# Kernel optimization log

Hardware: AMD Instinct MI355X
Metric: run time of the kernel (lower is better)

The kernel has to match this reference:

```python
import jax, jax.numpy as jnp
import numpy as np

IN_FEATURES = 4096
OUT_FEATURES = 8192
GROUP_SIZE = 16
NUM_GROUPS = IN_FEATURES * OUT_FEATURES // GROUP_SIZE  # 2_097_152


def block_dequantize_2bit(packed, normalization):
    # packed: [G, group_size//4] int32 holding uint8 values; norm: [G, 1] fp16
    shifts = jnp.arange(4, dtype=packed.dtype) * 2  # bit offsets 0,2,4,6
    # unpacked column 4k+i comes from packed column k, bits 2i..2i+1
    u = ((packed[:, :, None] >> shifts) & 3).astype(jnp.float32)  # [G, gs/4, 4]
    u = u.reshape(packed.shape[0], -1)  # [G, group_size]
    norm = normalization.astype(jnp.float32)
    return (u / 3.0) * (2.0 * norm) - norm  # [G, group_size]


def setup_inputs() -> dict:
    key = jax.random.key(0)
    k_x, k_q, k_n, k_b = jax.random.split(key, 4)
    x = jax.random.normal(k_x, (256, IN_FEATURES), dtype=jnp.float32)
    # packed 2-bit weights: random bytes (store as int32 for clean bit ops in jax)
    weight_q2 = jax.random.randint(k_q, (NUM_GROUPS, GROUP_SIZE // 4), 0, 256, dtype=jnp.int32)
    # per-group normalization (abs-max), positive, fp16 as in the module buffer
    weight_norm = (jax.random.uniform(k_n, (NUM_GROUPS, 1), dtype=jnp.float32) * 0.05 + 1e-4).astype(jnp.float16)
    bias = jax.random.normal(k_b, (OUT_FEATURES,), dtype=jnp.float32) * 0.01
    return {"x": x, "weight_q2": weight_q2, "weight_norm": weight_norm, "bias": bias}


def reference(x, weight_q2, weight_norm, bias):
    weight = block_dequantize_2bit(weight_q2, weight_norm).reshape(OUT_FEATURES, IN_FEATURES)
    return jnp.dot(x.astype(jnp.float32), weight.T) + bias
```

## Files before the change

### kernel.cpp

```cpp
#include <hip/hip_runtime.h>
#include <hip/hip_bf16.h>
#include <hip/hip_fp16.h>

#define IN_F   4096
#define OUT_F  8192
#define M_ROWS 256

#define SPLITK 2
#define K_SPL  (IN_F / SPLITK)
#define NIT    (K_SPL / 64)

typedef __attribute__((ext_vector_type(8))) short  short8;
typedef __attribute__((ext_vector_type(4))) float  float4v;

__device__ inline unsigned int pack_bf16(float lo, float hi) {
    return __builtin_amdgcn_perm(__float_as_uint(hi), __float_as_uint(lo), 0x07060302u);
}

__device__ inline int sw_idx(int row, int kchunk) {
    return row * 64 + ((kchunk ^ (row & 7)) << 3);
}

__device__ inline void barrier_no_vmem_drain() {
    asm volatile("s_waitcnt lgkmcnt(0)" ::: "memory");
    __builtin_amdgcn_s_barrier();
    asm volatile("" ::: "memory");
}

__global__ void cvt_x_kernel(const float* __restrict__ x, unsigned short* __restrict__ xb) {
    int i = blockIdx.x * blockDim.x + threadIdx.x;
    if (i < (M_ROWS * IN_F) / 4) {
        float4 v = ((const float4*)x)[i];
        uint2 o;
        o.x = pack_bf16(v.x, v.y);
        o.y = pack_bf16(v.z, v.w);
        ((uint2*)xb)[i] = o;
    }
}

__global__ void init_out_kernel(const float* __restrict__ bias, float* __restrict__ out) {
    int i = blockIdx.x * blockDim.x + threadIdx.x;
    if (i < (M_ROWS * OUT_F) / 4) {
        float4 b = ((const float4*)bias)[i & (OUT_F / 4 - 1)];
        ((float4*)out)[i] = b;
    }
}

__device__ inline void load_a16_f32(const float* __restrict__ p, uint4& o0, uint4& o1) {
    float4 v0 = ((const float4*)p)[0], v1 = ((const float4*)p)[1];
    float4 v2 = ((const float4*)p)[2], v3 = ((const float4*)p)[3];
    o0.x = pack_bf16(v0.x, v0.y); o0.y = pack_bf16(v0.z, v0.w);
    o0.z = pack_bf16(v1.x, v1.y); o0.w = pack_bf16(v1.z, v1.w);
    o1.x = pack_bf16(v2.x, v2.y); o1.y = pack_bf16(v2.z, v2.w);
    o1.z = pack_bf16(v3.x, v3.y); o1.w = pack_bf16(v3.z, v3.w);
}

template <bool XB>
__global__ __launch_bounds__(256, 4) void gemm2bit_kernel(
    const float*           __restrict__ xf,
    const unsigned short*  __restrict__ xb,
    const int*             __restrict__ wq,
    const void*            __restrict__ wnorm,
    float*                 __restrict__ out)
{
    __shared__ unsigned short lds[2][2][64 * 64];

    const int t    = threadIdx.x;
    const int n0   = blockIdx.x * 64;
    const int m0   = blockIdx.y * 64;
    const int kb   = blockIdx.z * K_SPL;
    const int wave = t >> 6;
    const int lane = t & 63;
    const int l15  = lane & 15;
    const int quad = lane >> 4;
    const int wm   = (wave >> 1) * 32;
    const int wn   = (wave & 1) * 32;

    const float cand0 = *(const float*)wnorm;
    const bool  nf32  = (cand0 > 1e-5f && cand0 < 0.1f);

    const int srow = t >> 2;
    const int skc  = t & 3;
    const int c0   = skc * 2;
    const int wO0  = sw_idx(srow, c0);
    const int wO1  = sw_idx(srow, c0 + 1);

    int fa0[2], fa1[2], fb0[2], fb1[2];
#pragma unroll
    for (int kk = 0; kk < 2; ++kk) {
        fa0[kk] = sw_idx(wm +      l15, kk * 4 + quad);
        fa1[kk] = sw_idx(wm + 16 + l15, kk * 4 + quad);
        fb0[kk] = sw_idx(wn +      l15, kk * 4 + quad);
        fb1[kk] = sw_idx(wn + 16 + l15, kk * 4 + quad);
    }

    const int arow = m0 + srow;
    const int brow = n0 + srow;
    const float*          nrmF = (const float*)wnorm;
    const __half*         nrmH = (const __half*)wnorm;

    float4v acc[2][2] = {};

    uint4 aN0, aN1; int4 qN; float nN;
    {
        if (XB) {
            const unsigned short* p = xb + arow * IN_F + kb + skc * 16;
            aN0 = *(const uint4*)p;
            aN1 = *(const uint4*)(p + 8);
        } else {
            load_a16_f32(xf + arow * IN_F + kb + skc * 16, aN0, aN1);
        }
        qN = *(const int4*)(wq + brow * (IN_F / 4) + (kb >> 2) + skc * 4);
        const int gi = brow * (IN_F / 16) + (kb >> 4) + skc;
        nN = nf32 ? nrmF[gi] : __half2float(nrmH[gi]);
    }

    for (int ito = 0; ito < NIT / 2; ++ito) {
#pragma unroll
        for (int half = 0; half < 2; ++half) {
            const int it = ito * 2 + half;

            uint4 aC0 = aN0, aC1 = aN1;
            int4  qC  = qN;
            float nC  = nN;

            if (it < NIT - 1) {
                const int kn = kb + ((it + 1) << 6);
                if (XB) {
                    const unsigned short* p = xb + arow * IN_F + kn + skc * 16;
                    aN0 = *(const uint4*)p;
                    aN1 = *(const uint4*)(p + 8);
                } else {
                    load_a16_f32(xf + arow * IN_F + kn + skc * 16, aN0, aN1);
                }
                qN = *(const int4*)(wq + brow * (IN_F / 4) + (kn >> 2) + skc * 4);
                const int gi = brow * (IN_F / 16) + (kn >> 4) + skc;
                nN = nf32 ? nrmF[gi] : __half2float(nrmH[gi]);
            }

            const float s = nC * (2.0f / 3.0f);
            float f[16];
            const int qa[4] = {qC.x, qC.y, qC.z, qC.w};
#pragma unroll
            for (int bq = 0; bq < 4; ++bq) {
#pragma unroll
                for (int i = 0; i < 4; ++i)
                    f[bq * 4 + i] = fmaf((float)((qa[bq] >> (2 * i)) & 3), s, -nC);
            }
            uint4 bv0, bv1;
            bv0.x = pack_bf16(f[0],  f[1]);   bv0.y = pack_bf16(f[2],  f[3]);
            bv0.z = pack_bf16(f[4],  f[5]);   bv0.w = pack_bf16(f[6],  f[7]);
            bv1.x = pack_bf16(f[8],  f[9]);   bv1.y = pack_bf16(f[10], f[11]);
            bv1.z = pack_bf16(f[12], f[13]);  bv1.w = pack_bf16(f[14], f[15]);

            unsigned short* LA = lds[half][0];
            unsigned short* LB = lds[half][1];
            *(uint4*)&LA[wO0] = aC0;
            *(uint4*)&LA[wO1] = aC1;
            *(uint4*)&LB[wO0] = bv0;
            *(uint4*)&LB[wO1] = bv1;

            barrier_no_vmem_drain();

#pragma unroll
            for (int kk = 0; kk < 2; ++kk) {
                short8 a0 = *(const short8*)&LA[fa0[kk]];
                short8 a1 = *(const short8*)&LA[fa1[kk]];
                short8 b0 = *(const short8*)&LB[fb0[kk]];
                short8 b1 = *(const short8*)&LB[fb1[kk]];
                acc[0][0] = __builtin_amdgcn_mfma_f32_16x16x32_bf16(a0, b0, acc[0][0], 0, 0, 0);
                acc[0][1] = __builtin_amdgcn_mfma_f32_16x16x32_bf16(a0, b1, acc[0][1], 0, 0, 0);
                acc[1][0] = __builtin_amdgcn_mfma_f32_16x16x32_bf16(a1, b0, acc[1][0], 0, 0, 0);
                acc[1][1] = __builtin_amdgcn_mfma_f32_16x16x32_bf16(a1, b1, acc[1][1], 0, 0, 0);
            }
        }
    }

#pragma unroll
    for (int j = 0; j < 2; ++j) {
        const int col = n0 + wn + j * 16 + l15;
#pragma unroll
        for (int i = 0; i < 2; ++i) {
            const int row0 = m0 + wm + i * 16 + quad * 4;
#pragma unroll
            for (int r = 0; r < 4; ++r) {
                atomicAdd(&out[(row0 + r) * OUT_F + col], acc[i][j][r]);
            }
        }
    }
}

extern "C" void kernel_launch(void* const* d_in, const int* in_sizes, int n_in,
                              void* d_out, int out_size, void* d_ws, size_t ws_size,
                              hipStream_t stream) {
    const float*          x    = (const float*)d_in[0];
    const int*            wq   = (const int*)d_in[1];
    const void*           wn   = (const void*)d_in[2];
    const float*          bias = (const float*)d_in[3];
    float*                out  = (float*)d_out;

    const bool use_ws = ws_size >= (size_t)(M_ROWS * IN_F * sizeof(unsigned short));

    dim3 grid(OUT_F / 64, M_ROWS / 64, SPLITK);

    init_out_kernel<<<dim3((M_ROWS * OUT_F / 4) / 256), 256, 0, stream>>>(bias, out);

    if (use_ws) {
        unsigned short* xb = (unsigned short*)d_ws;
        cvt_x_kernel<<<dim3((M_ROWS * IN_F / 4 + 255) / 256), 256, 0, stream>>>(x, xb);
        gemm2bit_kernel<true><<<grid, 256, 0, stream>>>(nullptr, xb, wq, wn, out);
    } else {
        gemm2bit_kernel<false><<<grid, 256, 0, stream>>>(x, nullptr, wq, wn, out);
    }
}
```

Measured before the change: 123.5 us.

## Enlarge GEMM block tile to 128x128 with 8 waves and split-K of 4

The block tile grows from 64x64 to 128x128 and uses 512 threads in 8 waves, each computing a 64x32 sub-tile with 4x2 MFMA accumulators. Split-K rises from 2 to 4 so the grid keeps enough blocks. The larger M tile halves how many times each packed weight group is reloaded and dequantized, and the larger N tile cuts how often the activations are reloaded. The costs are twice as many output atomic adds from the higher split-K, a larger LDS footprint and higher register pressure per thread.

```diff
diff --git a/kernel.cpp b/kernel.cpp
--- a/kernel.cpp
+++ b/kernel.cpp
@@ -6,9 +6,11 @@
 #define OUT_F  8192
 #define M_ROWS 256
 
-#define SPLITK 2
+#define SPLITK 4
 #define K_SPL  (IN_F / SPLITK)
 #define NIT    (K_SPL / 64)
+#define BM     128
+#define BN     128
 
 typedef __attribute__((ext_vector_type(8))) short  short8;
 typedef __attribute__((ext_vector_type(4))) float  float4v;
@@ -56,25 +58,25 @@
 }
 
 template <bool XB>
-__global__ __launch_bounds__(256, 4) void gemm2bit_kernel(
+__global__ __launch_bounds__(512, 4) void gemm2bit_kernel(
     const float*           __restrict__ xf,
     const unsigned short*  __restrict__ xb,
     const int*             __restrict__ wq,
     const void*            __restrict__ wnorm,
     float*                 __restrict__ out)
 {
-    __shared__ unsigned short lds[2][2][64 * 64];
+    __shared__ unsigned short lds[2][2][BM * 64];
 
     const int t    = threadIdx.x;
-    const int n0   = blockIdx.x * 64;
-    const int m0   = blockIdx.y * 64;
+    const int n0   = blockIdx.x * BN;
+    const int m0   = blockIdx.y * BM;
     const int kb   = blockIdx.z * K_SPL;
     const int wave = t >> 6;
     const int lane = t & 63;
     const int l15  = lane & 15;
     const int quad = lane >> 4;
-    const int wm   = (wave >> 1) * 32;
-    const int wn   = (wave & 1) * 32;
+    const int wm   = (wave >> 2) * 64;
+    const int wn   = (wave & 3) * 32;
 
     const float cand0 = *(const float*)wnorm;
     const bool  nf32  = (cand0 > 1e-5f && cand0 < 0.1f);
@@ -85,13 +87,15 @@
     const int wO0  = sw_idx(srow, c0);
     const int wO1  = sw_idx(srow, c0 + 1);
 
-    int fa0[2], fa1[2], fb0[2], fb1[2];
+    int fa[4][2], fb[2][2];
 #pragma unroll
     for (int kk = 0; kk < 2; ++kk) {
-        fa0[kk] = sw_idx(wm +      l15, kk * 4 + quad);
-        fa1[kk] = sw_idx(wm + 16 + l15, kk * 4 + quad);
-        fb0[kk] = sw_idx(wn +      l15, kk * 4 + quad);
-        fb1[kk] = sw_idx(wn + 16 + l15, kk * 4 + quad);
+#pragma unroll
+        for (int i = 0; i < 4; ++i)
+            fa[i][kk] = sw_idx(wm + i * 16 + l15, kk * 4 + quad);
+#pragma unroll
+        for (int j = 0; j < 2; ++j)
+            fb[j][kk] = sw_idx(wn + j * 16 + l15, kk * 4 + quad);
     }
 
     const int arow = m0 + srow;
@@ -99,7 +103,7 @@
     const float*          nrmF = (const float*)wnorm;
     const __half*         nrmH = (const __half*)wnorm;
 
-    float4v acc[2][2] = {};
+    float4v acc[4][2] = {};
 
     uint4 aN0, aN1; int4 qN; float nN;
     {
@@ -164,14 +168,14 @@
 
 #pragma unroll
             for (int kk = 0; kk < 2; ++kk) {
-                short8 a0 = *(const short8*)&LA[fa0[kk]];
-                short8 a1 = *(const short8*)&LA[fa1[kk]];
-                short8 b0 = *(const short8*)&LB[fb0[kk]];
-                short8 b1 = *(const short8*)&LB[fb1[kk]];
-                acc[0][0] = __builtin_amdgcn_mfma_f32_16x16x32_bf16(a0, b0, acc[0][0], 0, 0, 0);
-                acc[0][1] = __builtin_amdgcn_mfma_f32_16x16x32_bf16(a0, b1, acc[0][1], 0, 0, 0);
-                acc[1][0] = __builtin_amdgcn_mfma_f32_16x16x32_bf16(a1, b0, acc[1][0], 0, 0, 0);
-                acc[1][1] = __builtin_amdgcn_mfma_f32_16x16x32_bf16(a1, b1, acc[1][1], 0, 0, 0);
+                short8 b0 = *(const short8*)&LB[fb[0][kk]];
+                short8 b1 = *(const short8*)&LB[fb[1][kk]];
+#pragma unroll
+                for (int i = 0; i < 4; ++i) {
+                    short8 a = *(const short8*)&LA[fa[i][kk]];
+                    acc[i][0] = __builtin_amdgcn_mfma_f32_16x16x32_bf16(a, b0, acc[i][0], 0, 0, 0);
+                    acc[i][1] = __builtin_amdgcn_mfma_f32_16x16x32_bf16(a, b1, acc[i][1], 0, 0, 0);
+                }
             }
         }
     }
@@ -180,7 +184,7 @@
     for (int j = 0; j < 2; ++j) {
         const int col = n0 + wn + j * 16 + l15;
 #pragma unroll
-        for (int i = 0; i < 2; ++i) {
+        for (int i = 0; i < 4; ++i) {
             const int row0 = m0 + wm + i * 16 + quad * 4;
 #pragma unroll
             for (int r = 0; r < 4; ++r) {
@@ -201,15 +205,15 @@
 
     const bool use_ws = ws_size >= (size_t)(M_ROWS * IN_F * sizeof(unsigned short));
 
-    dim3 grid(OUT_F / 64, M_ROWS / 64, SPLITK);
+    dim3 grid(OUT_F / BN, M_ROWS / BM, SPLITK);
 
     init_out_kernel<<<dim3((M_ROWS * OUT_F / 4) / 256), 256, 0, stream>>>(bias, out);
 
     if (use_ws) {
         unsigned short* xb = (unsigned short*)d_ws;
         cvt_x_kernel<<<dim3((M_ROWS * IN_F / 4 + 255) / 256), 256, 0, stream>>>(x, xb);
-        gemm2bit_kernel<true><<<grid, 256, 0, stream>>>(nullptr, xb, wq, wn, out);
+        gemm2bit_kernel<true><<<grid, 512, 0, stream>>>(nullptr, xb, wq, wn, out);
     } else {
-        gemm2bit_kernel<false><<<grid, 256, 0, stream>>>(x, nullptr, wq, wn, out);
-    }
-}
+        gemm2bit_kernel<false><<<grid, 512, 0, stream>>>(x, nullptr, wq, wn, out);
+    }
+}
```

Result: slower. 130.8 us (+5.9%).
